# Kernel optimization log

Hardware: AMD Instinct MI355X
Metric: run time of the kernel (lower is better)

The kernel has to match this reference:

```python
import jax, jax.numpy as jnp
import numpy as np

NUM_HEADS = 16
N_EMBED = 1024
HEAD_SIZE = 64
BLOCK_SIZE = 2048


def setup_inputs() -> dict:
    key = jax.random.key(0)
    ks = jax.random.split(key, 6)
    B, S, C, H, D = 2, BLOCK_SIZE, N_EMBED, NUM_HEADS, HEAD_SIZE
    x = jax.random.normal(ks[0], (B, S, C), dtype=jnp.float32)
    scale = C ** -0.5
    # per-head q/k/v projections (bias=False), stacked over heads: [H, C, D]
    Wq = jax.random.normal(ks[1], (H, C, D), dtype=jnp.float32) * scale
    Wk = jax.random.normal(ks[2], (H, C, D), dtype=jnp.float32) * scale
    Wv = jax.random.normal(ks[3], (H, C, D), dtype=jnp.float32) * scale
    # output projection Linear(H*D, C)
    Wo = jax.random.normal(ks[4], (H * D, C), dtype=jnp.float32) * ((H * D) ** -0.5)
    bo = jax.random.normal(ks[5], (C,), dtype=jnp.float32) * 0.01
    return {"x": x, "Wq": Wq, "Wk": Wk, "Wv": Wv, "Wo": Wo, "bo": bo}


def reference(x, Wq, Wk, Wv, Wo, bo):
    B, S, C = x.shape
    H, _, D = Wq.shape
    # project: [B, H, S, D]
    q = jnp.einsum("bsc,hcd->bhsd", x, Wq)
    k = jnp.einsum("bsc,hcd->bhsd", x, Wk)
    v = jnp.einsum("bsc,hcd->bhsd", x, Wv)
    # scaled causal attention scores: [B, H, S, S]
    scores = jnp.einsum("bhsd,bhtd->bhst", q, k) * (D ** -0.5)
    causal = jnp.tril(jnp.ones((S, S), dtype=bool))
    scores = jnp.where(causal, scores, jnp.finfo(scores.dtype).min)
    attn = jax.nn.softmax(scores, axis=-1)
    out = jnp.einsum("bhst,bhtd->bhsd", attn, v)  # [B, H, S, D]
    # concat heads -> [B, S, H*D], then output projection
    out = out.transpose(0, 2, 1, 3).reshape(B, S, H * D)
    return out @ Wo + bo
```

## Files before the change

kernel.cpp:

```cpp
#include <hip/hip_runtime.h>
#include <cstdint>
#include <cstddef>

constexpr int SEQ  = 2048;
constexpr int CH   = 1024;
constexpr int NH   = 16;
constexpr int HS   = 64;
constexpr int NB   = 2;
constexpr int HDIM = NH * HS;

typedef __bf16 bf16x8 __attribute__((ext_vector_type(8)));
typedef __bf16 bf16x4 __attribute__((ext_vector_type(4)));
typedef float  f32x4  __attribute__((ext_vector_type(4)));

__device__ __forceinline__ unsigned short f2bf(float f) {
  union { float f; unsigned u; } v; v.f = f;
  unsigned u = v.u;
  u += 0x7fffu + ((u >> 16) & 1u);
  return (unsigned short)(u >> 16);
}
__device__ __forceinline__ float bf2f(unsigned short h) {
  union { unsigned u; float f; } v; v.u = ((unsigned)h) << 16;
  return v.f;
}
__device__ __forceinline__ float load_elem(const void* p, int flag, size_t idx) {
  if (flag) return ((const float*)p)[idx];
  return bf2f(((const unsigned short*)p)[idx]);
}
__device__ __forceinline__ void gl_lds16(const unsigned short* g, unsigned short* l) {
  __builtin_amdgcn_global_load_lds(
      (const __attribute__((address_space(1))) unsigned int*)g,
      (__attribute__((address_space(3))) unsigned int*)l, 16, 0, 0);
}

__device__ int detect_flag_block(const void* p, int n, int tid, int nthr) {
  __shared__ int det_good;
  if (tid == 0) det_good = 0;
  __syncthreads();
  const unsigned short* u = (const unsigned short*)p;
  int good = 0;
  for (int j = tid; j < n; j += nthr) {
    unsigned short v = u[2 * j];
    int e = (v >> 7) & 0xFF;
    if (v != 0 && e >= 90 && e <= 150) good++;
  }
  atomicAdd(&det_good, good);
  __syncthreads();
  return (det_good * 10 >= n * 7) ? 0 : 1;
}

__global__ __launch_bounds__(256) void prep(
    const void* __restrict__ x,  const void* __restrict__ wq,
    const void* __restrict__ wk, const void* __restrict__ wv,
    const void* __restrict__ wo,
    unsigned short* __restrict__ xb,
    unsigned short* __restrict__ wall,
    unsigned short* __restrict__ wot) {
  __shared__ unsigned short tile[32][36];
  int idx = blockIdx.x, tid = threadIdx.x;
  int row = tid >> 3, cg = (tid & 7) * 4;
  int col = tid >> 3, rg = (tid & 7) * 4;
  if (idx < 1024) {
    int f = detect_flag_block(x, 512, tid, 256);
    size_t n4 = (size_t)NB * SEQ * CH / 4;
    for (size_t i = (size_t)idx * 256 + tid; i < n4; i += (size_t)1024 * 256) {
      ushort4 o;
      if (f) {
        float4 v = ((const float4*)x)[i];
        o.x = f2bf(v.x); o.y = f2bf(v.y); o.z = f2bf(v.z); o.w = f2bf(v.w);
      } else {
        o = ((const ushort4*)x)[i];
      }
      ((ushort4*)xb)[i] = o;
    }
  } else if (idx < 4096) {
    int j = idx - 1024;
    int which = j >> 10, hh = (j >> 6) & 15, sub = j & 63;
    const void* src = (which == 0) ? wq : (which == 1) ? wk : wv;
    int f = detect_flag_block(src, 512, tid, 256);
    int c0 = (sub & 1) * 32;
    int r0 = (sub >> 1) * 32;
    size_t boff = (size_t)hh * CH * HS;
    size_t si = boff + (size_t)(r0 + row) * HS + c0 + cg;
    ushort4 t4;
    if (f) {
      float4 v = *(const float4*)((const float*)src + si);
      t4.x = f2bf(v.x); t4.y = f2bf(v.y); t4.z = f2bf(v.z); t4.w = f2bf(v.w);
    } else {
      t4 = *(const ushort4*)((const unsigned short*)src + si);
    }
    *(ushort4*)&tile[row][cg] = t4;
    __syncthreads();
    unsigned short* d = wall + ((size_t)which * NH + hh) * HS * CH;
    ushort4 o;
    o.x = tile[rg + 0][col]; o.y = tile[rg + 1][col];
    o.z = tile[rg + 2][col]; o.w = tile[rg + 3][col];
    *(ushort4*)&d[(size_t)(c0 + col) * CH + r0 + rg] = o;
  } else {
    int sub = idx - 4096;
    int f = detect_flag_block(wo, 512, tid, 256);
    int c0 = (sub & 31) * 32;
    int r0 = (sub >> 5) * 32;
    size_t si = (size_t)(r0 + row) * CH + c0 + cg;
    ushort4 t4;
    if (f) {
      float4 v = *(const float4*)((const float*)wo + si);
      t4.x = f2bf(v.x); t4.y = f2bf(v.y); t4.z = f2bf(v.z); t4.w = f2bf(v.w);
    } else {
      t4 = *(const ushort4*)((const unsigned short*)wo + si);
    }
    *(ushort4*)&tile[row][cg] = t4;
    __syncthreads();
    ushort4 o;
    o.x = tile[rg + 0][col]; o.y = tile[rg + 1][col];
    o.z = tile[rg + 2][col]; o.w = tile[rg + 3][col];
    *(ushort4*)&wot[(size_t)(c0 + col) * HDIM + r0 + rg] = o;
  }
}

__global__ __launch_bounds__(256) void qkv_gemm(
    const unsigned short* __restrict__ xb,
    const unsigned short* __restrict__ wall,
    unsigned short* __restrict__ qo,
    unsigned short* __restrict__ ko,
    unsigned short* __restrict__ vt) {
  __shared__ __attribute__((aligned(16))) unsigned short Al[128 * 64];
  __shared__ __attribute__((aligned(16))) unsigned short Bl[128 * 64];
  int mt = blockIdx.x, nt = blockIdx.y;
  const unsigned short* A  = xb   + (size_t)mt * 128 * CH;
  const unsigned short* Bm = wall + (size_t)nt * 128 * CH;
  int tid = threadIdx.x, wave = tid >> 6, lane = tid & 63;
  int quad = lane >> 4, l15 = lane & 15;
  int r8 = lane >> 3, c8 = lane & 7;
  int gcol = ((c8 ^ r8) << 3);
  int x7 = l15 & 7;
  int wm = (wave >> 1) * 64, wn = (wave & 1) * 64;
  f32x4 acc[4][4];
  #pragma unroll
  for (int i = 0; i < 4; i++)
    #pragma unroll
    for (int j = 0; j < 4; j++) acc[i][j] = (f32x4){0.f, 0.f, 0.f, 0.f};

  for (int k0 = 0; k0 < CH; k0 += 64) {
    #pragma unroll
    for (int c = 0; c < 4; c++) {
      int row = wave * 32 + c * 8 + r8;
      gl_lds16(&A [(size_t)row * CH + k0 + gcol], &Al[(wave * 32 + c * 8) * 64]);
      gl_lds16(&Bm[(size_t)row * CH + k0 + gcol], &Bl[(wave * 32 + c * 8) * 64]);
    }
    __syncthreads();
    #pragma unroll
    for (int h = 0; h < 2; h++) {
      int cq = ((quad + 4 * h) ^ x7) << 3;
      bf16x8 af[4], bfr[4];
      #pragma unroll
      for (int fm = 0; fm < 4; fm++)
        af[fm] = *reinterpret_cast<const bf16x8*>(&Al[(wm + fm * 16 + l15) * 64 + cq]);
      #pragma unroll
      for (int fn = 0; fn < 4; fn++)
        bfr[fn] = *reinterpret_cast<const bf16x8*>(&Bl[(wn + fn * 16 + l15) * 64 + cq]);
      #pragma unroll
      for (int fm = 0; fm < 4; fm++)
        #pragma unroll
        for (int fn = 0; fn < 4; fn++)
          acc[fm][fn] = __builtin_amdgcn_mfma_f32_16x16x32_bf16(af[fm], bfr[fn], acc[fm][fn], 0, 0, 0);
    }
    __syncthreads();
  }

  int seg = (nt * 128) >> 10;
  int nb  = (nt * 128) & 1023;
  if (seg < 2) {
    unsigned short* dst = (seg == 0) ? qo : ko;
    float s = (seg == 0) ? 0.18033688011112042f : 1.0f;
    #pragma unroll
    for (int fn = 0; fn < 4; fn++) {
      int c = nb + wn + fn * 16 + l15, h = c >> 6, d = c & 63;
      #pragma unroll
      for (int fm = 0; fm < 4; fm++) {
        int m = mt * 128 + wm + fm * 16 + quad * 4;
        int b = m >> 11, s0 = m & 2047;
        #pragma unroll
        for (int r = 0; r < 4; r++)
          dst[(((size_t)b * NH + h) * SEQ + s0 + r) * HS + d] = f2bf(acc[fm][fn][r] * s);
      }
    }
  } else {
    #pragma unroll
    for (int fn = 0; fn < 4; fn++) {
      int c = nb + wn + fn * 16 + l15, h = c >> 6, d = c & 63;
      #pragma unroll
      for (int fm = 0; fm < 4; fm++) {
        int m = mt * 128 + wm + fm * 16 + quad * 4;
        int b = m >> 11, s0 = m & 2047;
        ushort4 pk;
        pk.x = f2bf(acc[fm][fn][0]); pk.y = f2bf(acc[fm][fn][1]);
        pk.z = f2bf(acc[fm][fn][2]); pk.w = f2bf(acc[fm][fn][3]);
        *(ushort4*)&vt[(((size_t)b * NH + h) * HS + d) * SEQ + s0] = pk;
      }
    }
  }
}

template <bool MASKED>
__device__ __forceinline__ void soft_pack(const f32x4* s, f32x4& ls,
                                          unsigned short* ptRow, int quad, int tmb) {
  #pragma unroll
  for (int tb = 0; tb < 4; tb++) {
    f32x4 pv;
    #pragma unroll
    for (int r = 0; r < 4; r++) {
      float p = __builtin_amdgcn_exp2f(s[tb][r]);
      if (MASKED) { if (tmb + tb * 16 + quad * 4 + r > 0) p = 0.f; }
      pv[r] = p;
    }
    ls += pv;
    bf16x4 pk;
    pk.x = (__bf16)pv[0]; pk.y = (__bf16)pv[1];
    pk.z = (__bf16)pv[2]; pk.w = (__bf16)pv[3];
    *(bf16x4*)&ptRow[tb * 16 + quad * 4] = pk;
  }
}

template <int QKM, bool PV0, bool PVV>
__device__ __forceinline__ void attn_step(
    const unsigned short (&Kb)[64][64], const unsigned short (&Vp)[64][64],
    unsigned short* p0row, unsigned short* p1row,
    const bf16x8 (&qf)[2][2], f32x4 (&lsum)[2], f32x4 (&accO)[2][4],
    bf16x8 (&bq0)[2], bf16x8 (&bq1)[2],
    int quad, int l15, int tmb) {
  constexpr bool C0 = (QKM <= 1);
  constexpr bool M0 = (QKM == 1);
  constexpr bool M1 = (QKM == 3);
  int x7 = l15 & 7;
  f32x4 s0[4], s1[4];
  #pragma unroll
  for (int tb = 0; tb < 4; tb++) { s0[tb] = (f32x4){0,0,0,0}; s1[tb] = (f32x4){0,0,0,0}; }
  __builtin_amdgcn_s_setprio(1);
  #pragma unroll
  for (int tb = 0; tb < 4; tb++)
    #pragma unroll
    for (int hh = 0; hh < 2; hh++) {
      bf16x8 kf = *reinterpret_cast<const bf16x8*>(
          &Kb[tb * 16 + l15][((hh * 4 + quad) ^ x7) << 3]);
      if (C0) s0[tb] = __builtin_amdgcn_mfma_f32_16x16x32_bf16(kf, qf[0][hh], s0[tb], 0, 0, 0);
      s1[tb] = __builtin_amdgcn_mfma_f32_16x16x32_bf16(kf, qf[1][hh], s1[tb], 0, 0, 0);
    }
  if (PVV) {
    #pragma unroll
    for (int db = 0; db < 4; db++)
      #pragma unroll
      for (int tp = 0; tp < 2; tp++) {
        bf16x8 vf = *reinterpret_cast<const bf16x8*>(
            &Vp[db * 16 + l15][((tp * 4 + quad) ^ x7) << 3]);
        if (PV0) accO[0][db] = __builtin_amdgcn_mfma_f32_16x16x32_bf16(vf, bq0[tp], accO[0][db], 0, 0, 0);
        accO[1][db] = __builtin_amdgcn_mfma_f32_16x16x32_bf16(vf, bq1[tp], accO[1][db], 0, 0, 0);
      }
  }
  __builtin_amdgcn_s_setprio(0);
  if (C0) soft_pack<M0>(s0, lsum[0], p0row, quad, tmb);
  soft_pack<M1>(s1, lsum[1], p1row, quad, tmb);
  #pragma unroll
  for (int tp = 0; tp < 2; tp++) {
    if (C0) bq0[tp] = *reinterpret_cast<const bf16x8*>(&p0row[tp * 32 + quad * 8]);
    bq1[tp] = *reinterpret_cast<const bf16x8*>(&p1row[tp * 32 + quad * 8]);
  }
}

__global__ __launch_bounds__(256) void attn_k(
    const unsigned short* __restrict__ q,
    const unsigned short* __restrict__ k,
    const unsigned short* __restrict__ vt,
    unsigned short* __restrict__ y) {
  __shared__ __attribute__((aligned(16))) unsigned short Kl[3][64][64];
  __shared__ __attribute__((aligned(16))) unsigned short Vl[3][64][64];
  __shared__ __attribute__((aligned(16))) unsigned short Pt[4][16][152];

  int p = blockIdx.x;
  int st0 = p, st1 = 31 - p;
  int bh = blockIdx.y, b = bh >> 4, h = bh & 15;
  const unsigned short* Q0 = q + ((size_t)bh * SEQ + st0 * 64) * HS;
  const unsigned short* Q1 = q + ((size_t)bh * SEQ + st1 * 64) * HS;
  const unsigned short* K  = k  + (size_t)bh * SEQ * HS;
  const unsigned short* V  = vt + (size_t)bh * HS * SEQ;
  int tid = threadIdx.x, wave = tid >> 6, lane = tid & 63;
  int quad = lane >> 4, l15 = lane & 15;
  int lr = tid >> 3, lc = (tid & 7) * 8;
  int sc = (((tid & 7) ^ (lr & 7)) << 3);

  bf16x8 qf[2][2];
  #pragma unroll
  for (int hh = 0; hh < 2; hh++) {
    qf[0][hh] = *reinterpret_cast<const bf16x8*>(
        &Q0[(size_t)(wave * 16 + l15) * HS + hh * 32 + quad * 8]);
    qf[1][hh] = *reinterpret_cast<const bf16x8*>(
        &Q1[(size_t)(wave * 16 + l15) * HS + hh * 32 + quad * 8]);
  }

  f32x4 lsum[2] = {(f32x4){0,0,0,0}, (f32x4){0,0,0,0}};
  f32x4 accO[2][4];
  #pragma unroll
  for (int f = 0; f < 2; f++)
    #pragma unroll
    for (int i = 0; i < 4; i++) accO[f][i] = (f32x4){0.f, 0.f, 0.f, 0.f};
  bf16x8 bq0[2], bq1[2];

  unsigned short* p0row = &Pt[wave][l15][0];
  unsigned short* p1row = &Pt[wave][l15][64];
  int tmb = -(wave * 16 + l15);

  uint4 kr0, kr1, vr0, vr1;
  auto g2r = [&](int kv) {
    kr0 = *(const uint4*)&K[(size_t)(kv * 64 + lr) * HS + lc];
    kr1 = *(const uint4*)&K[(size_t)(kv * 64 + lr + 32) * HS + lc];
    vr0 = *(const uint4*)&V[(size_t)lr * SEQ + kv * 64 + lc];
    vr1 = *(const uint4*)&V[(size_t)(lr + 32) * SEQ + kv * 64 + lc];
  };
  auto r2l = [&](int nb) {
    *(uint4*)&Kl[nb][lr][sc] = kr0; *(uint4*)&Kl[nb][lr + 32][sc] = kr1;
    *(uint4*)&Vl[nb][lr][sc] = vr0; *(uint4*)&Vl[nb][lr + 32][sc] = vr1;
  };

  g2r(0); r2l(0);
  __syncthreads();

  {
    if (st1 > 0) g2r(1);
    if (st0 == 0)
      attn_step<1, false, false>(Kl[0], Vl[2], p0row, p1row, qf, lsum, accO, bq0, bq1, quad, l15, tmb);
    else
      attn_step<0, false, false>(Kl[0], Vl[2], p0row, p1row, qf, lsum, accO, bq0, bq1, quad, l15, tmb);
    if (st1 > 0) r2l(1);
    __syncthreads();
  }
  for (int t = 1; t < st0; t++) {
    g2r(t + 1);
    attn_step<0, true, true>(Kl[t % 3], Vl[(t + 2) % 3], p0row, p1row, qf, lsum, accO, bq0, bq1, quad, l15, tmb);
    r2l((t + 1) % 3);
    __syncthreads();
  }
  if (st0 >= 1) {
    int t = st0;
    g2r(t + 1);
    attn_step<1, true, true>(Kl[t % 3], Vl[(t + 2) % 3], p0row, p1row, qf, lsum, accO, bq0, bq1, quad, l15, tmb);
    r2l((t + 1) % 3);
    __syncthreads();
  }
  {
    int t = st0 + 1;
    bool more = (t < st1);
    if (more) g2r(t + 1);
    if (t == st1)
      attn_step<3, true, true>(Kl[t % 3], Vl[(t + 2) % 3], p0row, p1row, qf, lsum, accO, bq0, bq1, quad, l15, tmb);
    else
      attn_step<2, true, true>(Kl[t % 3], Vl[(t + 2) % 3], p0row, p1row, qf, lsum, accO, bq0, bq1, quad, l15, tmb);
    if (more) r2l((t + 1) % 3);
    __syncthreads();
  }
  for (int t = st0 + 2; t < st1; t++) {
    g2r(t + 1);
    attn_step<2, false, true>(Kl[t % 3], Vl[(t + 2) % 3], p0row, p1row, qf, lsum, accO, bq0, bq1, quad, l15, tmb);
    r2l((t + 1) % 3);
    __syncthreads();
  }
  if (st1 >= st0 + 2) {
    int t = st1;
    attn_step<3, false, true>(Kl[t % 3], Vl[(t + 2) % 3], p0row, p1row, qf, lsum, accO, bq0, bq1, quad, l15, tmb);
  }
  {
    const unsigned short (&Vb)[64][64] = Vl[st1 % 3];
    int x7 = l15 & 7;
    #pragma unroll
    for (int db = 0; db < 4; db++)
      #pragma unroll
      for (int tp = 0; tp < 2; tp++) {
        bf16x8 vf = *reinterpret_cast<const bf16x8*>(
            &Vb[db * 16 + l15][((tp * 4 + quad) ^ x7) << 3]);
        accO[1][db] = __builtin_amdgcn_mfma_f32_16x16x32_bf16(vf, bq1[tp], accO[1][db], 0, 0, 0);
      }
  }

  #pragma unroll
  for (int f = 0; f < 2; f++) {
    float rs = (lsum[f][0] + lsum[f][1]) + (lsum[f][2] + lsum[f][3]);
    rs += __shfl_xor(rs, 16); rs += __shfl_xor(rs, 32);
    float inv = 1.0f / fmaxf(rs, 1e-30f);
    int srow = (f == 0 ? st0 : st1) * 64 + wave * 16 + l15;
    #pragma unroll
    for (int db = 0; db < 4; db++) {
      ushort4 pk;
      pk.x = f2bf(accO[f][db][0] * inv); pk.y = f2bf(accO[f][db][1] * inv);
      pk.z = f2bf(accO[f][db][2] * inv); pk.w = f2bf(accO[f][db][3] * inv);
      *(ushort4*)&y[((size_t)b * SEQ + srow) * HDIM + h * 64 + db * 16 + quad * 4] = pk;
    }
  }
}

__global__ __launch_bounds__(256) void out_gemm(
    const unsigned short* __restrict__ y,
    const unsigned short* __restrict__ wot,
    const void* __restrict__ bo,
    float* __restrict__ out) {
  __shared__ __attribute__((aligned(16))) unsigned short Al[128 * 64];
  __shared__ __attribute__((aligned(16))) unsigned short Bl[64 * 64];
  int tid = threadIdx.x;
  int fbo = detect_flag_block(bo, 512, tid, 256);
  int mt = blockIdx.x, nt = blockIdx.y;
  const unsigned short* A  = y   + (size_t)mt * 128 * HDIM;
  const unsigned short* Bm = wot + (size_t)nt * 64 * HDIM;
  int wave = tid >> 6, lane = tid & 63;
  int quad = lane >> 4, l15 = lane & 15;
  int r8 = lane >> 3, c8 = lane & 7;
  int gcol = ((c8 ^ r8) << 3);
  int x7 = l15 & 7;
  int wm = (wave >> 1) * 64, wn = (wave & 1) * 32;
  f32x4 acc[4][2];
  #pragma unroll
  for (int i = 0; i < 4; i++)
    #pragma unroll
    for (int j = 0; j < 2; j++) acc[i][j] = (f32x4){0.f, 0.f, 0.f, 0.f};

  for (int k0 = 0; k0 < HDIM; k0 += 64) {
    #pragma unroll
    for (int c = 0; c < 4; c++) {
      int row = wave * 32 + c * 8 + r8;
      gl_lds16(&A[(size_t)row * HDIM + k0 + gcol], &Al[(wave * 32 + c * 8) * 64]);
    }
    #pragma unroll
    for (int c = 0; c < 2; c++) {
      int row = wave * 16 + c * 8 + r8;
      gl_lds16(&Bm[(size_t)row * HDIM + k0 + gcol], &Bl[(wave * 16 + c * 8) * 64]);
    }
    __syncthreads();
    #pragma unroll
    for (int h = 0; h < 2; h++) {
      int cq = ((quad + 4 * h) ^ x7) << 3;
      bf16x8 af[4], bfr[2];
      #pragma unroll
      for (int fm = 0; fm < 4; fm++)
        af[fm] = *reinterpret_cast<const bf16x8*>(&Al[(wm + fm * 16 + l15) * 64 + cq]);
      #pragma unroll
      for (int fn = 0; fn < 2; fn++)
        bfr[fn] = *reinterpret_cast<const bf16x8*>(&Bl[(wn + fn * 16 + l15) * 64 + cq]);
      #pragma unroll
      for (int fm = 0; fm < 4; fm++)
        #pragma unroll
        for (int fn = 0; fn < 2; fn++)
          acc[fm][fn] = __builtin_amdgcn_mfma_f32_16x16x32_bf16(af[fm], bfr[fn], acc[fm][fn], 0, 0, 0);
    }
    __syncthreads();
  }

  #pragma unroll
  for (int fn = 0; fn < 2; fn++) {
    int n = nt * 64 + wn + fn * 16 + l15;
    float bias = load_elem(bo, fbo, n);
    #pragma unroll
    for (int fm = 0; fm < 4; fm++) {
      int m = mt * 128 + wm + fm * 16 + quad * 4;
      #pragma unroll
      for (int r = 0; r < 4; r++)
        out[(size_t)(m + r) * CH + n] = acc[fm][fn][r] + bias;
    }
  }
}

extern "C" void kernel_launch(void* const* d_in, const int* in_sizes, int n_in,
                              void* d_out, int out_size, void* d_ws, size_t ws_size,
                              hipStream_t stream) {
  const void* x  = d_in[0];
  const void* Wq = d_in[1];
  const void* Wk = d_in[2];
  const void* Wv = d_in[3];
  const void* Wo = d_in[4];
  const void* bo = d_in[5];
  float* out = (float*)d_out;

  char* ws = (char*)d_ws;
  const size_t MB = 1024 * 1024;
  unsigned short* qb   = (unsigned short*)(ws + 0);
  unsigned short* kb   = (unsigned short*)(ws + 8  * MB);
  unsigned short* vtb  = (unsigned short*)(ws + 16 * MB);
  unsigned short* yb   = (unsigned short*)(ws + 24 * MB);
  unsigned short* wall = (unsigned short*)(ws + 32 * MB);
  unsigned short* wot  = (unsigned short*)(ws + 38 * MB);
  unsigned short* xb   = (unsigned short*)(ws + 40 * MB);

  prep<<<5120, 256, 0, stream>>>(x, Wq, Wk, Wv, Wo, xb, wall, wot);
  qkv_gemm<<<dim3(NB * SEQ / 128, 3 * HDIM / 128), 256, 0, stream>>>(xb, wall, qb, kb, vtb);
  attn_k<<<dim3(16, NB * NH), 256, 0, stream>>>(qb, kb, vtb, yb);
  out_gemm<<<dim3(NB * SEQ / 128, CH / 64), 256, 0, stream>>>(yb, wot, bo, out);
}
```

Measured before the change: 187.6 us.

## Double-buffer QKV GEMM LDS tiles and widen N tile to 192

The QKV projection GEMM now double-buffers its LDS tiles, prefetching the next K slice while MFMAs run on the current one, which removes one barrier per iteration. The N tile grows from 128 to 192 columns, giving 4x6 accumulators per wave and 512 blocks instead of 768, and s_setprio raises wave priority around the MFMA burst. The epilogue now picks the Q, K or V target per 16-column fragment because a 192-wide tile can straddle segments. This costs more LDS (80KB per block), more registers, and a grid that may fill the CUs unevenly.

```diff
diff --git a/kernel.cpp b/kernel.cpp
--- a/kernel.cpp
+++ b/kernel.cpp
@@ -118,64 +118,77 @@
   }
 }
 
-__global__ __launch_bounds__(256) void qkv_gemm(
+__global__ __launch_bounds__(256, 2) void qkv_gemm(
     const unsigned short* __restrict__ xb,
     const unsigned short* __restrict__ wall,
     unsigned short* __restrict__ qo,
     unsigned short* __restrict__ ko,
     unsigned short* __restrict__ vt) {
-  __shared__ __attribute__((aligned(16))) unsigned short Al[128 * 64];
-  __shared__ __attribute__((aligned(16))) unsigned short Bl[128 * 64];
+  __shared__ __attribute__((aligned(16))) unsigned short Al[2][128 * 64];
+  __shared__ __attribute__((aligned(16))) unsigned short Bl[2][192 * 64];
   int mt = blockIdx.x, nt = blockIdx.y;
   const unsigned short* A  = xb   + (size_t)mt * 128 * CH;
-  const unsigned short* Bm = wall + (size_t)nt * 128 * CH;
+  const unsigned short* Bm = wall + (size_t)nt * 192 * CH;
   int tid = threadIdx.x, wave = tid >> 6, lane = tid & 63;
   int quad = lane >> 4, l15 = lane & 15;
   int r8 = lane >> 3, c8 = lane & 7;
   int gcol = ((c8 ^ r8) << 3);
   int x7 = l15 & 7;
-  int wm = (wave >> 1) * 64, wn = (wave & 1) * 64;
-  f32x4 acc[4][4];
+  int wm = (wave >> 1) * 64, wn = (wave & 1) * 96;
+  f32x4 acc[4][6];
   #pragma unroll
   for (int i = 0; i < 4; i++)
     #pragma unroll
-    for (int j = 0; j < 4; j++) acc[i][j] = (f32x4){0.f, 0.f, 0.f, 0.f};
-
-  for (int k0 = 0; k0 < CH; k0 += 64) {
+    for (int j = 0; j < 6; j++) acc[i][j] = (f32x4){0.f, 0.f, 0.f, 0.f};
+
+  auto stage = [&](int bb, int k0) {
     #pragma unroll
     for (int c = 0; c < 4; c++) {
       int row = wave * 32 + c * 8 + r8;
-      gl_lds16(&A [(size_t)row * CH + k0 + gcol], &Al[(wave * 32 + c * 8) * 64]);
-      gl_lds16(&Bm[(size_t)row * CH + k0 + gcol], &Bl[(wave * 32 + c * 8) * 64]);
-    }
-    __syncthreads();
+      gl_lds16(&A[(size_t)row * CH + k0 + gcol], &Al[bb][(wave * 32 + c * 8) * 64]);
+    }
+    #pragma unroll
+    for (int c = 0; c < 6; c++) {
+      int row = wave * 48 + c * 8 + r8;
+      gl_lds16(&Bm[(size_t)row * CH + k0 + gcol], &Bl[bb][(wave * 48 + c * 8) * 64]);
+    }
+  };
+
+  stage(0, 0);
+  __syncthreads();
+  for (int ks = 0; ks < 16; ks++) {
+    int bb = ks & 1;
+    if (ks < 15) stage(bb ^ 1, (ks + 1) * 64);
     #pragma unroll
     for (int h = 0; h < 2; h++) {
       int cq = ((quad + 4 * h) ^ x7) << 3;
-      bf16x8 af[4], bfr[4];
+      bf16x8 af[4], bfr[6];
       #pragma unroll
       for (int fm = 0; fm < 4; fm++)
-        af[fm] = *reinterpret_cast<const bf16x8*>(&Al[(wm + fm * 16 + l15) * 64 + cq]);
-      #pragma unroll
-      for (int fn = 0; fn < 4; fn++)
-        bfr[fn] = *reinterpret_cast<const bf16x8*>(&Bl[(wn + fn * 16 + l15) * 64 + cq]);
+        af[fm] = *reinterpret_cast<const bf16x8*>(&Al[bb][(wm + fm * 16 + l15) * 64 + cq]);
+      #pragma unroll
+      for (int fn = 0; fn < 6; fn++)
+        bfr[fn] = *reinterpret_cast<const bf16x8*>(&Bl[bb][(wn + fn * 16 + l15) * 64 + cq]);
+      __builtin_amdgcn_s_setprio(1);
       #pragma unroll
       for (int fm = 0; fm < 4; fm++)
         #pragma unroll
-        for (int fn = 0; fn < 4; fn++)
+        for (int fn = 0; fn < 6; fn++)
           acc[fm][fn] = __builtin_amdgcn_mfma_f32_16x16x32_bf16(af[fm], bfr[fn], acc[fm][fn], 0, 0, 0);
-    }
-    __syncthreads();
-  }
-
-  int seg = (nt * 128) >> 10;
-  int nb  = (nt * 128) & 1023;
-  if (seg < 2) {
-    unsigned short* dst = (seg == 0) ? qo : ko;
-    float s = (seg == 0) ? 0.18033688011112042f : 1.0f;
-    #pragma unroll
-    for (int fn = 0; fn < 4; fn++) {
-      int c = nb + wn + fn * 16 + l15, h = c >> 6, d = c & 63;
+      __builtin_amdgcn_s_setprio(0);
+    }
+    __syncthreads();
+  }
+
+  #pragma unroll
+  for (int fn = 0; fn < 6; fn++) {
+    int c0 = nt * 192 + wn + fn * 16;
+    int seg = c0 >> 10;
+    int hd = (c0 & 1023) + l15;
+    int h = hd >> 6, d = hd & 63;
+    if (seg < 2) {
+      unsigned short* dst = (seg == 0) ? qo : ko;
+      float s = (seg == 0) ? 0.18033688011112042f : 1.0f;
       #pragma unroll
       for (int fm = 0; fm < 4; fm++) {
         int m = mt * 128 + wm + fm * 16 + quad * 4;
@@ -184,11 +197,7 @@
         for (int r = 0; r < 4; r++)
           dst[(((size_t)b * NH + h) * SEQ + s0 + r) * HS + d] = f2bf(acc[fm][fn][r] * s);
       }
-    }
-  } else {
-    #pragma unroll
-    for (int fn = 0; fn < 4; fn++) {
-      int c = nb + wn + fn * 16 + l15, h = c >> 6, d = c & 63;
+    } else {
       #pragma unroll
       for (int fm = 0; fm < 4; fm++) {
         int m = mt * 128 + wm + fm * 16 + quad * 4;
@@ -487,7 +496,7 @@
   unsigned short* xb   = (unsigned short*)(ws + 40 * MB);
 
   prep<<<5120, 256, 0, stream>>>(x, Wq, Wk, Wv, Wo, xb, wall, wot);
-  qkv_gemm<<<dim3(NB * SEQ / 128, 3 * HDIM / 128), 256, 0, stream>>>(xb, wall, qb, kb, vtb);
+  qkv_gemm<<<dim3(NB * SEQ / 128, 3 * HDIM / 192), 256, 0, stream>>>(xb, wall, qb, kb, vtb);
   attn_k<<<dim3(16, NB * NH), 256, 0, stream>>>(qb, kb, vtb, yb);
   out_gemm<<<dim3(NB * SEQ / 128, CH / 64), 256, 0, stream>>>(yb, wot, bo, out);
 }
```

Measured after the change: 176.5 us. 5.9% less time.
